# Performance work log

Hardware: AMD Instinct MI355X
Metric: run time of the kernel (lower is better)

## Reference

```python
import jax, jax.numpy as jnp
import numpy as np

DIM = 768
N_HEADS = 12
HEAD_DIM = DIM // N_HEADS
B, T = 2, 2048


def setup_inputs() -> dict:
    key = jax.random.key(0)
    ks = jax.random.split(key, 11)
    s = 0.02
    return {
        "q_in": jax.random.normal(ks[0], (B, T, DIM), jnp.float32),
        "k_in": jax.random.normal(ks[1], (B, T, DIM), jnp.float32),
        "v_in": jax.random.normal(ks[2], (B, T, DIM), jnp.float32),
        "Wq": jax.random.normal(ks[3], (DIM, DIM), jnp.float32) * s,
        "bq": jnp.zeros((DIM,), jnp.float32),
        "Wk": jax.random.normal(ks[4], (DIM, DIM), jnp.float32) * s,
        "bk": jnp.zeros((DIM,), jnp.float32),
        "Wv": jax.random.normal(ks[5], (DIM, DIM), jnp.float32) * s,
        "bv": jnp.zeros((DIM,), jnp.float32),
        "Wo": jax.random.normal(ks[6], (DIM, DIM), jnp.float32) * s,
        "bo": jnp.zeros((DIM,), jnp.float32),
    }


def reference(q_in, k_in, v_in, Wq, bq, Wk, bk, Wv, bv, Wo, bo):
    b, t, c = q_in.shape
    scale = HEAD_DIM ** -0.5
    # linear projections (torch Linear: x @ W.T + b)
    q = q_in @ Wq.T + bq
    k = k_in @ Wk.T + bk
    v = v_in @ Wv.T + bv
    # [b, t, h, d] -> [b, h, t, d]
    q = q.reshape(b, t, N_HEADS, HEAD_DIM).transpose(0, 2, 1, 3)
    k = k.reshape(b, t, N_HEADS, HEAD_DIM).transpose(0, 2, 1, 3)
    v = v.reshape(b, t, N_HEADS, HEAD_DIM).transpose(0, 2, 1, 3)
    scores = jnp.einsum("bhqd,bhkd->bhqk", q, k) * scale  # full TxT scores
    probs = jax.nn.softmax(scores, axis=-1)
    attn = jnp.einsum("bhqk,bhkd->bhqd", probs, v)
    attn = attn.transpose(0, 2, 1, 3).reshape(b, t, c)
    return attn @ Wo.T + bo
```

## Files before the change

### kernel.cpp

```cpp
#include <hip/hip_runtime.h>


typedef unsigned short u16;
typedef __attribute__((ext_vector_type(8))) short short8;
typedef __attribute__((ext_vector_type(4))) float float4v;

#define DIMC 768
#define NTOK 4096
#define NHD  12
#define HDD  64
#define SEQT 2048

__device__ __forceinline__ u16 f2bf(float f) {
  union { float f; unsigned u; } v; v.f = f;
  unsigned r = v.u + 0x7fffu + ((v.u >> 16) & 1u);
  return (u16)(r >> 16);
}
__device__ __forceinline__ float bf2f(u16 u) {
  union { unsigned u; float f; } v; v.u = ((unsigned)u) << 16;
  return v.f;
}

__global__ __launch_bounds__(256) void cvt3_kernel(
    const float* __restrict__ a, const float* __restrict__ b, const float* __restrict__ c,
    u16* __restrict__ oa, u16* __restrict__ ob, u16* __restrict__ oc) {
  int z = blockIdx.y;
  const float* s = (z == 0) ? a : (z == 1) ? b : c;
  u16* d = (z == 0) ? oa : (z == 1) ? ob : oc;
  size_t i = ((size_t)blockIdx.x * 256 + threadIdx.x) * 4;
  float4 v = *(const float4*)(s + i);
  *(ushort4*)(d + i) = make_ushort4(f2bf(v.x), f2bf(v.y), f2bf(v.z), f2bf(v.w));
}

__global__ __launch_bounds__(256) void cvt4_kernel(
    const float* __restrict__ a, const float* __restrict__ b,
    const float* __restrict__ c, const float* __restrict__ e,
    u16* __restrict__ oa, u16* __restrict__ ob, u16* __restrict__ oc, u16* __restrict__ oe) {
  int z = blockIdx.y;
  const float* s = (z == 0) ? a : (z == 1) ? b : (z == 2) ? c : e;
  u16* d = (z == 0) ? oa : (z == 1) ? ob : (z == 2) ? oc : oe;
  size_t i = ((size_t)blockIdx.x * 256 + threadIdx.x) * 4;
  float4 v = *(const float4*)(s + i);
  *(ushort4*)(d + i) = make_ushort4(f2bf(v.x), f2bf(v.y), f2bf(v.z), f2bf(v.w));
}

__device__ __forceinline__ void gemm_mainloop2(
    const u16* __restrict__ X, const u16* __restrict__ W,
    int m0, int n0, u16* Als, u16* Bls, float4v acc[4][2]) {
  int tid = threadIdx.x;
  int sr = tid >> 3, sc = (tid & 7) * 8;
  int w = tid >> 6, lane = tid & 63, quad = lane >> 4, r15 = lane & 15;
  int wm = (w >> 1) * 64, wn = (w & 1) * 32;
  const u16* xp0 = X + (size_t)(m0 + sr) * DIMC + sc;
  const u16* xp1 = xp0 + 32 * DIMC;
  const u16* xp2 = xp0 + 64 * DIMC;
  const u16* xp3 = xp0 + 96 * DIMC;
  const u16* wp0 = W + (size_t)(n0 + sr) * DIMC + sc;
  const u16* wp1 = wp0 + 32 * DIMC;
  uint4 pa0 = *(const uint4*)xp0, pa1 = *(const uint4*)xp1;
  uint4 pa2 = *(const uint4*)xp2, pa3 = *(const uint4*)xp3;
  uint4 pb0 = *(const uint4*)wp0, pb1 = *(const uint4*)wp1;
  for (int k0 = 0; k0 < DIMC; k0 += 64) {
    __syncthreads();
    *(uint4*)(Als + sr * 72 + sc) = pa0;
    *(uint4*)(Als + (sr + 32) * 72 + sc) = pa1;
    *(uint4*)(Als + (sr + 64) * 72 + sc) = pa2;
    *(uint4*)(Als + (sr + 96) * 72 + sc) = pa3;
    *(uint4*)(Bls + sr * 72 + sc) = pb0;
    *(uint4*)(Bls + (sr + 32) * 72 + sc) = pb1;
    __syncthreads();
    int kn = k0 + 64;
    if (kn < DIMC) {
      pa0 = *(const uint4*)(xp0 + kn); pa1 = *(const uint4*)(xp1 + kn);
      pa2 = *(const uint4*)(xp2 + kn); pa3 = *(const uint4*)(xp3 + kn);
      pb0 = *(const uint4*)(wp0 + kn); pb1 = *(const uint4*)(wp1 + kn);
    }
    #pragma unroll
    for (int sk = 0; sk < 2; sk++) {
      short8 af[4], bf[2];
      #pragma unroll
      for (int mf = 0; mf < 4; mf++)
        af[mf] = *(const short8*)(Als + (wm + mf * 16 + r15) * 72 + sk * 32 + quad * 8);
      #pragma unroll
      for (int nf = 0; nf < 2; nf++)
        bf[nf] = *(const short8*)(Bls + (wn + nf * 16 + r15) * 72 + sk * 32 + quad * 8);
      #pragma unroll
      for (int mf = 0; mf < 4; mf++)
        #pragma unroll
        for (int nf = 0; nf < 2; nf++)
          acc[mf][nf] = __builtin_amdgcn_mfma_f32_16x16x32_bf16(af[mf], bf[nf], acc[mf][nf], 0, 0, 0);
    }
  }
}

__global__ __launch_bounds__(256, 4) void gemm_qkv(
    const u16* __restrict__ xq, const u16* __restrict__ xk, const u16* __restrict__ xv,
    const u16* __restrict__ wq, const u16* __restrict__ wk, const u16* __restrict__ wv,
    const float* __restrict__ bq, const float* __restrict__ bk, const float* __restrict__ bv,
    u16* __restrict__ Qh, u16* __restrict__ Kh, u16* __restrict__ Vt) {
  __shared__ __align__(16) u16 Als[128 * 72];
  __shared__ __align__(16) u16 Bls[64 * 72];
  int z = blockIdx.z;
  const u16* X = (z == 0) ? xq : (z == 1) ? xk : xv;
  const u16* W = (z == 0) ? wq : (z == 1) ? wk : wv;
  const float* bias = (z == 0) ? bq : (z == 1) ? bk : bv;
  int m0 = blockIdx.x * 128, n0 = blockIdx.y * 64;
  float4v acc[4][2];
  #pragma unroll
  for (int i = 0; i < 4; i++)
    #pragma unroll
    for (int j = 0; j < 2; j++)
      #pragma unroll
      for (int r = 0; r < 4; r++) acc[i][j][r] = 0.f;
  gemm_mainloop2(X, W, m0, n0, Als, Bls, acc);
  int tid = threadIdx.x, w = tid >> 6, lane = tid & 63, quad = lane >> 4, r15 = lane & 15;
  int wm = (w >> 1) * 64, wn = (w & 1) * 32;
  #pragma unroll
  for (int mf = 0; mf < 4; mf++)
    #pragma unroll
    for (int nf = 0; nf < 2; nf++)
      #pragma unroll
      for (int rg = 0; rg < 4; rg++) {
        int m = m0 + wm + mf * 16 + quad * 4 + rg;
        int n = n0 + wn + nf * 16 + r15;
        float val = acc[mf][nf][rg] + bias[n];
        int b = m >> 11, t = m & 2047, h = n >> 6, d = n & 63;
        u16 o = f2bf(val);
        size_t bh = (size_t)(b * NHD + h);
        if (z == 2) Vt[(bh * HDD + d) * SEQT + t] = o;
        else if (z == 0) Qh[(bh * SEQT + t) * HDD + d] = o;
        else Kh[(bh * SEQT + t) * HDD + d] = o;
      }
}

__global__ __launch_bounds__(256, 3) void attn_kernel(
    const u16* __restrict__ Qh, const u16* __restrict__ Kh, const u16* __restrict__ Vt,
    u16* __restrict__ Opart, float* __restrict__ Lpart) {
  constexpr float CEXP = 0.125f * 1.44269504088896f;
  __shared__ __align__(16) u16 Kls[64 * 72];
  __shared__ __align__(16) u16 Vls[64 * 72];
  __shared__ __align__(16) u16 Pls[4 * 32 * 72];
  int bh = blockIdx.y, kv = blockIdx.z, qt0 = blockIdx.x * 128;
  int tid = threadIdx.x, w = tid >> 6, lane = tid & 63, quad = lane >> 4, r15 = lane & 15;
  int qw = qt0 + w * 32;

  short8 qa[2][2];
  #pragma unroll
  for (int qs = 0; qs < 2; qs++) {
    const u16* qp = Qh + ((size_t)bh * SEQT + qw + qs * 16 + r15) * HDD + quad * 8;
    qa[qs][0] = *(const short8*)qp;
    qa[qs][1] = *(const short8*)(qp + 32);
  }
  short8 ones;
  #pragma unroll
  for (int i = 0; i < 8; i++) ones[i] = (short)0x3F80;

  float4v oacc[2][4], lacc[2];
  #pragma unroll
  for (int qs = 0; qs < 2; qs++) {
    #pragma unroll
    for (int r = 0; r < 4; r++) lacc[qs][r] = 0.f;
    #pragma unroll
    for (int dt = 0; dt < 4; dt++)
      #pragma unroll
      for (int r = 0; r < 4; r++) oacc[qs][dt][r] = 0.f;
  }

  const u16* Kbase = Kh + (size_t)bh * SEQT * HDD;
  const u16* Vbase = Vt + (size_t)bh * HDD * SEQT;
  u16* Pw = Pls + w * (32 * 72);
  int sr = tid >> 3, sc = (tid & 7) * 8;
  int kt0 = kv * 1024;

  uint4 pk0 = *(const uint4*)(Kbase + (size_t)(kt0 + sr) * HDD + sc);
  uint4 pk1 = *(const uint4*)(Kbase + (size_t)(kt0 + sr + 32) * HDD + sc);
  uint4 pv0 = *(const uint4*)(Vbase + (size_t)sr * SEQT + kt0 + sc);
  uint4 pv1 = *(const uint4*)(Vbase + (size_t)(sr + 32) * SEQT + kt0 + sc);

  for (int it = 0; it < 16; it++) {
    __syncthreads();
    *(uint4*)(Kls + sr * 72 + sc) = pk0;
    *(uint4*)(Kls + (sr + 32) * 72 + sc) = pk1;
    *(uint4*)(Vls + sr * 72 + sc) = pv0;
    *(uint4*)(Vls + (sr + 32) * 72 + sc) = pv1;
    __syncthreads();
    int ktn = kt0 + ((it + 1) & 15) * 64;
    pk0 = *(const uint4*)(Kbase + (size_t)(ktn + sr) * HDD + sc);
    pk1 = *(const uint4*)(Kbase + (size_t)(ktn + sr + 32) * HDD + sc);
    pv0 = *(const uint4*)(Vbase + (size_t)sr * SEQT + ktn + sc);
    pv1 = *(const uint4*)(Vbase + (size_t)(sr + 32) * SEQT + ktn + sc);

    float4v st[4][2];
    #pragma unroll
    for (int nk = 0; nk < 4; nk++) {
      short8 k0 = *(const short8*)(Kls + (nk * 16 + r15) * 72 + quad * 8);
      short8 k1 = *(const short8*)(Kls + (nk * 16 + r15) * 72 + 32 + quad * 8);
      #pragma unroll
      for (int qs = 0; qs < 2; qs++) {
        float4v z;
        #pragma unroll
        for (int r = 0; r < 4; r++) z[r] = 0.f;
        z = __builtin_amdgcn_mfma_f32_16x16x32_bf16(k0, qa[qs][0], z, 0, 0, 0);
        z = __builtin_amdgcn_mfma_f32_16x16x32_bf16(k1, qa[qs][1], z, 0, 0, 0);
        st[nk][qs] = z;
      }
    }
    #pragma unroll
    for (int qs = 0; qs < 2; qs++)
      #pragma unroll
      for (int nk = 0; nk < 4; nk++) {
        float p0 = exp2f(st[nk][qs][0] * CEXP);
        float p1 = exp2f(st[nk][qs][1] * CEXP);
        float p2 = exp2f(st[nk][qs][2] * CEXP);
        float p3 = exp2f(st[nk][qs][3] * CEXP);
        unsigned lo = __builtin_amdgcn_perm(__float_as_uint(p1), __float_as_uint(p0), 0x07060302u);
        unsigned hi = __builtin_amdgcn_perm(__float_as_uint(p3), __float_as_uint(p2), 0x07060302u);
        *(uint2*)(Pw + (qs * 16 + r15) * 72 + nk * 16 + quad * 4) = make_uint2(lo, hi);
      }
    short8 pa[2][2];
    #pragma unroll
    for (int qs = 0; qs < 2; qs++) {
      pa[qs][0] = *(const short8*)(Pw + (qs * 16 + r15) * 72 + quad * 8);
      pa[qs][1] = *(const short8*)(Pw + (qs * 16 + r15) * 72 + 32 + quad * 8);
      lacc[qs] = __builtin_amdgcn_mfma_f32_16x16x32_bf16(pa[qs][0], ones, lacc[qs], 0, 0, 0);
      lacc[qs] = __builtin_amdgcn_mfma_f32_16x16x32_bf16(pa[qs][1], ones, lacc[qs], 0, 0, 0);
    }
    #pragma unroll
    for (int dt = 0; dt < 4; dt++) {
      short8 v0 = *(const short8*)(Vls + (dt * 16 + r15) * 72 + quad * 8);
      short8 v1 = *(const short8*)(Vls + (dt * 16 + r15) * 72 + 32 + quad * 8);
      #pragma unroll
      for (int qs = 0; qs < 2; qs++) {
        oacc[qs][dt] = __builtin_amdgcn_mfma_f32_16x16x32_bf16(pa[qs][0], v0, oacc[qs][dt], 0, 0, 0);
        oacc[qs][dt] = __builtin_amdgcn_mfma_f32_16x16x32_bf16(pa[qs][1], v1, oacc[qs][dt], 0, 0, 0);
      }
    }
  }
  size_t obase = ((size_t)kv * 2 * NHD + bh) * SEQT;
  #pragma unroll
  for (int qs = 0; qs < 2; qs++)
    #pragma unroll
    for (int rg = 0; rg < 4; rg++) {
      int q = qw + qs * 16 + quad * 4 + rg;
      u16* orow = Opart + (obase + q) * HDD;
      #pragma unroll
      for (int dt = 0; dt < 4; dt++) orow[dt * 16 + r15] = f2bf(oacc[qs][dt][rg]);
      if (r15 == 0) Lpart[obase + q] = lacc[qs][rg];
    }
}

__global__ __launch_bounds__(256) void merge_kernel(
    const u16* __restrict__ Opart, const float* __restrict__ Lpart, u16* __restrict__ X2) {
  int tid = threadIdx.x;
  int row = blockIdx.x * 32 + (tid >> 3);
  int dcol = (tid & 7) * 8;
  int bh = row >> 11, t = row & 2047;
  size_t off1 = (size_t)row * HDD + dcol;
  size_t off2 = off1 + (size_t)2 * NHD * SEQT * HDD;
  ushort4 a0 = *(const ushort4*)(Opart + off1);
  ushort4 a1 = *(const ushort4*)(Opart + off1 + 4);
  ushort4 b0 = *(const ushort4*)(Opart + off2);
  ushort4 b1 = *(const ushort4*)(Opart + off2 + 4);
  float inv = 1.0f / (Lpart[row] + Lpart[row + 2 * NHD * SEQT]);
  int b = bh / NHD, h = bh % NHD;
  u16 o[8];
  o[0] = f2bf((bf2f(a0.x) + bf2f(b0.x)) * inv);
  o[1] = f2bf((bf2f(a0.y) + bf2f(b0.y)) * inv);
  o[2] = f2bf((bf2f(a0.z) + bf2f(b0.z)) * inv);
  o[3] = f2bf((bf2f(a0.w) + bf2f(b0.w)) * inv);
  o[4] = f2bf((bf2f(a1.x) + bf2f(b1.x)) * inv);
  o[5] = f2bf((bf2f(a1.y) + bf2f(b1.y)) * inv);
  o[6] = f2bf((bf2f(a1.z) + bf2f(b1.z)) * inv);
  o[7] = f2bf((bf2f(a1.w) + bf2f(b1.w)) * inv);
  *(uint4*)(X2 + ((size_t)b * SEQT + t) * DIMC + h * HDD + dcol) = *(uint4*)o;
}

__global__ __launch_bounds__(256, 4) void gemm_out(
    const u16* __restrict__ X2, const u16* __restrict__ wo,
    const float* __restrict__ bo, float* __restrict__ out) {
  __shared__ __align__(16) u16 Als[128 * 72];
  __shared__ __align__(16) u16 Bls[64 * 72];
  int m0 = blockIdx.x * 128, n0 = blockIdx.y * 64;
  float4v acc[4][2];
  #pragma unroll
  for (int i = 0; i < 4; i++)
    #pragma unroll
    for (int j = 0; j < 2; j++)
      #pragma unroll
      for (int r = 0; r < 4; r++) acc[i][j][r] = 0.f;
  gemm_mainloop2(X2, wo, m0, n0, Als, Bls, acc);
  int tid = threadIdx.x, w = tid >> 6, lane = tid & 63, quad = lane >> 4, r15 = lane & 15;
  int wm = (w >> 1) * 64, wn = (w & 1) * 32;
  #pragma unroll
  for (int mf = 0; mf < 4; mf++)
    #pragma unroll
    for (int nf = 0; nf < 2; nf++)
      #pragma unroll
      for (int rg = 0; rg < 4; rg++) {
        int m = m0 + wm + mf * 16 + quad * 4 + rg;
        int n = n0 + wn + nf * 16 + r15;
        out[(size_t)m * DIMC + n] = acc[mf][nf][rg] + bo[n];
      }
}

extern "C" void kernel_launch(void* const* d_in, const int* in_sizes, int n_in,
                              void* d_out, int out_size, void* d_ws, size_t ws_size,
                              hipStream_t stream) {
  const float* q_in = (const float*)d_in[0];
  const float* k_in = (const float*)d_in[1];
  const float* v_in = (const float*)d_in[2];
  const float* Wq = (const float*)d_in[3];
  const float* bq = (const float*)d_in[4];
  const float* Wk = (const float*)d_in[5];
  const float* bk = (const float*)d_in[6];
  const float* Wv = (const float*)d_in[7];
  const float* bv = (const float*)d_in[8];
  const float* Wo = (const float*)d_in[9];
  const float* bo = (const float*)d_in[10];

  const size_t NX = (size_t)NTOK * DIMC;
  const size_t NW = (size_t)DIMC * DIMC;
  u16* ws = (u16*)d_ws;
  u16* qb = ws;
  u16* kb = qb + NX;
  u16* vb = kb + NX;
  u16* wqb = vb + NX;
  u16* wkb = wqb + NW;
  u16* wvb = wkb + NW;
  u16* wob = wvb + NW;
  u16* Qh = wob + NW;
  u16* Kh = Qh + NX;
  u16* Vt = Kh + NX;
  u16* X2 = Vt + NX;
  u16* Opart = qb;
  float* Lpart = (float*)(ws + 2 * NX);

  cvt3_kernel<<<dim3(NX / 1024, 3), 256, 0, stream>>>(q_in, k_in, v_in, qb, kb, vb);
  cvt4_kernel<<<dim3(NW / 1024, 4), 256, 0, stream>>>(Wq, Wk, Wv, Wo, wqb, wkb, wvb, wob);
  gemm_qkv<<<dim3(NTOK / 128, DIMC / 64, 3), 256, 0, stream>>>(
      qb, kb, vb, wqb, wkb, wvb, bq, bk, bv, Qh, Kh, Vt);
  attn_kernel<<<dim3(SEQT / 128, 2 * NHD, 2), 256, 0, stream>>>(Qh, Kh, Vt, Opart, Lpart);
  merge_kernel<<<dim3(2 * NHD * SEQT / 32), 256, 0, stream>>>(Opart, Lpart, X2);
  gemm_out<<<dim3(NTOK / 128, DIMC / 64), 256, 0, stream>>>(X2, wob, bo, (float*)d_out);
}
```

Measured before the change: 200.3 us.

## Fold softmax scale into Q projection and double attention KV tile to 128

The Q projection epilogue now multiplies by scale*log2(e), so the attention kernel can call the raw hardware exp2 with no per-element multiply. The attention loop stages 128 keys per iteration instead of 64, halving the number of barriers and loop trips, and processes the tile in two 64-key halves. The P buffer is unchanged, and a shared zero accumulator replaces the per-iteration zeroing. This raises LDS use (bigger K and V tiles) and register pressure from more prefetch registers, which could reduce occupancy below the 3 blocks per CU requested in the launch bounds.

```diff
diff --git a/kernel.cpp b/kernel.cpp
--- a/kernel.cpp
+++ b/kernel.cpp
@@ -124,6 +124,7 @@
         int m = m0 + wm + mf * 16 + quad * 4 + rg;
         int n = n0 + wn + nf * 16 + r15;
         float val = acc[mf][nf][rg] + bias[n];
+        if (z == 0) val *= 0.180336880f;
         int b = m >> 11, t = m & 2047, h = n >> 6, d = n & 63;
         u16 o = f2bf(val);
         size_t bh = (size_t)(b * NHD + h);
@@ -136,9 +137,8 @@
 __global__ __launch_bounds__(256, 3) void attn_kernel(
     const u16* __restrict__ Qh, const u16* __restrict__ Kh, const u16* __restrict__ Vt,
     u16* __restrict__ Opart, float* __restrict__ Lpart) {
-  constexpr float CEXP = 0.125f * 1.44269504088896f;
-  __shared__ __align__(16) u16 Kls[64 * 72];
-  __shared__ __align__(16) u16 Vls[64 * 72];
+  __shared__ __align__(16) u16 Kls[128 * 72];
+  __shared__ __align__(16) u16 Vls[64 * 136];
   __shared__ __align__(16) u16 Pls[4 * 32 * 72];
   int bh = blockIdx.y, kv = blockIdx.z, qt0 = blockIdx.x * 128;
   int tid = threadIdx.x, w = tid >> 6, lane = tid & 63, quad = lane >> 4, r15 = lane & 15;
@@ -154,6 +154,9 @@
   short8 ones;
   #pragma unroll
   for (int i = 0; i < 8; i++) ones[i] = (short)0x3F80;
+  float4v fzero;
+  #pragma unroll
+  for (int r = 0; r < 4; r++) fzero[r] = 0.f;
 
   float4v oacc[2][4], lacc[2];
   #pragma unroll
@@ -169,70 +172,77 @@
   const u16* Kbase = Kh + (size_t)bh * SEQT * HDD;
   const u16* Vbase = Vt + (size_t)bh * HDD * SEQT;
   u16* Pw = Pls + w * (32 * 72);
-  int sr = tid >> 3, sc = (tid & 7) * 8;
+  int krow = tid >> 3, kcol = (tid & 7) * 8;
+  int vrow = tid >> 4, vcol = (tid & 15) * 8;
   int kt0 = kv * 1024;
 
-  uint4 pk0 = *(const uint4*)(Kbase + (size_t)(kt0 + sr) * HDD + sc);
-  uint4 pk1 = *(const uint4*)(Kbase + (size_t)(kt0 + sr + 32) * HDD + sc);
-  uint4 pv0 = *(const uint4*)(Vbase + (size_t)sr * SEQT + kt0 + sc);
-  uint4 pv1 = *(const uint4*)(Vbase + (size_t)(sr + 32) * SEQT + kt0 + sc);
-
-  for (int it = 0; it < 16; it++) {
+  uint4 pk[4], pv[4];
+  #pragma unroll
+  for (int p = 0; p < 4; p++) {
+    pk[p] = *(const uint4*)(Kbase + (size_t)(kt0 + krow + p * 32) * HDD + kcol);
+    pv[p] = *(const uint4*)(Vbase + (size_t)(vrow + p * 16) * SEQT + kt0 + vcol);
+  }
+
+  for (int it = 0; it < 8; it++) {
     __syncthreads();
-    *(uint4*)(Kls + sr * 72 + sc) = pk0;
-    *(uint4*)(Kls + (sr + 32) * 72 + sc) = pk1;
-    *(uint4*)(Vls + sr * 72 + sc) = pv0;
-    *(uint4*)(Vls + (sr + 32) * 72 + sc) = pv1;
+    #pragma unroll
+    for (int p = 0; p < 4; p++) {
+      *(uint4*)(Kls + (krow + p * 32) * 72 + kcol) = pk[p];
+      *(uint4*)(Vls + (vrow + p * 16) * 136 + vcol) = pv[p];
+    }
     __syncthreads();
-    int ktn = kt0 + ((it + 1) & 15) * 64;
-    pk0 = *(const uint4*)(Kbase + (size_t)(ktn + sr) * HDD + sc);
-    pk1 = *(const uint4*)(Kbase + (size_t)(ktn + sr + 32) * HDD + sc);
-    pv0 = *(const uint4*)(Vbase + (size_t)sr * SEQT + ktn + sc);
-    pv1 = *(const uint4*)(Vbase + (size_t)(sr + 32) * SEQT + ktn + sc);
-
-    float4v st[4][2];
-    #pragma unroll
-    for (int nk = 0; nk < 4; nk++) {
-      short8 k0 = *(const short8*)(Kls + (nk * 16 + r15) * 72 + quad * 8);
-      short8 k1 = *(const short8*)(Kls + (nk * 16 + r15) * 72 + 32 + quad * 8);
+    int ktn = kt0 + ((it + 1) & 7) * 128;
+    #pragma unroll
+    for (int p = 0; p < 4; p++) {
+      pk[p] = *(const uint4*)(Kbase + (size_t)(ktn + krow + p * 32) * HDD + kcol);
+      pv[p] = *(const uint4*)(Vbase + (size_t)(vrow + p * 16) * SEQT + ktn + vcol);
+    }
+
+    #pragma unroll
+    for (int h = 0; h < 2; h++) {
+      float4v st[4][2];
+      #pragma unroll
+      for (int nk = 0; nk < 4; nk++) {
+        const u16* kp = Kls + (h * 64 + nk * 16 + r15) * 72 + quad * 8;
+        short8 k0 = *(const short8*)kp;
+        short8 k1 = *(const short8*)(kp + 32);
+        #pragma unroll
+        for (int qs = 0; qs < 2; qs++) {
+          float4v z = __builtin_amdgcn_mfma_f32_16x16x32_bf16(k0, qa[qs][0], fzero, 0, 0, 0);
+          z = __builtin_amdgcn_mfma_f32_16x16x32_bf16(k1, qa[qs][1], z, 0, 0, 0);
+          st[nk][qs] = z;
+        }
+      }
+      #pragma unroll
+      for (int qs = 0; qs < 2; qs++)
+        #pragma unroll
+        for (int nk = 0; nk < 4; nk++) {
+          float p0 = __builtin_amdgcn_exp2f(st[nk][qs][0]);
+          float p1 = __builtin_amdgcn_exp2f(st[nk][qs][1]);
+          float p2 = __builtin_amdgcn_exp2f(st[nk][qs][2]);
+          float p3 = __builtin_amdgcn_exp2f(st[nk][qs][3]);
+          unsigned lo = __builtin_amdgcn_perm(__float_as_uint(p1), __float_as_uint(p0), 0x07060302u);
+          unsigned hi = __builtin_amdgcn_perm(__float_as_uint(p3), __float_as_uint(p2), 0x07060302u);
+          *(uint2*)(Pw + (qs * 16 + r15) * 72 + nk * 16 + quad * 4) = make_uint2(lo, hi);
+        }
+      short8 pa[2][2];
       #pragma unroll
       for (int qs = 0; qs < 2; qs++) {
-        float4v z;
+        pa[qs][0] = *(const short8*)(Pw + (qs * 16 + r15) * 72 + quad * 8);
+        pa[qs][1] = *(const short8*)(Pw + (qs * 16 + r15) * 72 + 32 + quad * 8);
+        lacc[qs] = __builtin_amdgcn_mfma_f32_16x16x32_bf16(pa[qs][0], ones, lacc[qs], 0, 0, 0);
+        lacc[qs] = __builtin_amdgcn_mfma_f32_16x16x32_bf16(pa[qs][1], ones, lacc[qs], 0, 0, 0);
+      }
+      #pragma unroll
+      for (int dt = 0; dt < 4; dt++) {
+        const u16* vp = Vls + (dt * 16 + r15) * 136 + h * 64 + quad * 8;
+        short8 v0 = *(const short8*)vp;
+        short8 v1 = *(const short8*)(vp + 32);
         #pragma unroll
-        for (int r = 0; r < 4; r++) z[r] = 0.f;
-        z = __builtin_amdgcn_mfma_f32_16x16x32_bf16(k0, qa[qs][0], z, 0, 0, 0);
-        z = __builtin_amdgcn_mfma_f32_16x16x32_bf16(k1, qa[qs][1], z, 0, 0, 0);
-        st[nk][qs] = z;
-      }
-    }
-    #pragma unroll
-    for (int qs = 0; qs < 2; qs++)
-      #pragma unroll
-      for (int nk = 0; nk < 4; nk++) {
-        float p0 = exp2f(st[nk][qs][0] * CEXP);
-        float p1 = exp2f(st[nk][qs][1] * CEXP);
-        float p2 = exp2f(st[nk][qs][2] * CEXP);
-        float p3 = exp2f(st[nk][qs][3] * CEXP);
-        unsigned lo = __builtin_amdgcn_perm(__float_as_uint(p1), __float_as_uint(p0), 0x07060302u);
-        unsigned hi = __builtin_amdgcn_perm(__float_as_uint(p3), __float_as_uint(p2), 0x07060302u);
-        *(uint2*)(Pw + (qs * 16 + r15) * 72 + nk * 16 + quad * 4) = make_uint2(lo, hi);
-      }
-    short8 pa[2][2];
-    #pragma unroll
-    for (int qs = 0; qs < 2; qs++) {
-      pa[qs][0] = *(const short8*)(Pw + (qs * 16 + r15) * 72 + quad * 8);
-      pa[qs][1] = *(const short8*)(Pw + (qs * 16 + r15) * 72 + 32 + quad * 8);
-      lacc[qs] = __builtin_amdgcn_mfma_f32_16x16x32_bf16(pa[qs][0], ones, lacc[qs], 0, 0, 0);
-      lacc[qs] = __builtin_amdgcn_mfma_f32_16x16x32_bf16(pa[qs][1], ones, lacc[qs], 0, 0, 0);
-    }
-    #pragma unroll
-    for (int dt = 0; dt < 4; dt++) {
-      short8 v0 = *(const short8*)(Vls + (dt * 16 + r15) * 72 + quad * 8);
-      short8 v1 = *(const short8*)(Vls + (dt * 16 + r15) * 72 + 32 + quad * 8);
-      #pragma unroll
-      for (int qs = 0; qs < 2; qs++) {
-        oacc[qs][dt] = __builtin_amdgcn_mfma_f32_16x16x32_bf16(pa[qs][0], v0, oacc[qs][dt], 0, 0, 0);
-        oacc[qs][dt] = __builtin_amdgcn_mfma_f32_16x16x32_bf16(pa[qs][1], v1, oacc[qs][dt], 0, 0, 0);
+        for (int qs = 0; qs < 2; qs++) {
+          oacc[qs][dt] = __builtin_amdgcn_mfma_f32_16x16x32_bf16(pa[qs][0], v0, oacc[qs][dt], 0, 0, 0);
+          oacc[qs][dt] = __builtin_amdgcn_mfma_f32_16x16x32_bf16(pa[qs][1], v1, oacc[qs][dt], 0, 0, 0);
+        }
       }
     }
   }
```

New measurement: 268.5 us. 34.1% more time.

## Split attention KV into three chunks, coalesce V transpose, fold softmax scale into Q

Applied to the files above, without the earlier changes.

The attention grid now splits the 32 key tiles into three uneven chunks (11/11/10) instead of two, with occupancy hint raised to 4, and the merge kernel sums three partials. The QKV GEMM stages the V tile through shared memory so the transposed Vt writes become 16-byte coalesced stores instead of scattered 2-byte ones. The softmax scale times log2(e) is folded into Q at projection time, so the attention kernel can call the raw exp2 builtin with no per-element multiply. The trade-offs are a wave-quantization change from the new grid size, extra partial traffic in merge, and Lpart relocated into the dead Wq buffer.

```diff
diff --git a/kernel.cpp b/kernel.cpp
--- a/kernel.cpp
+++ b/kernel.cpp
@@ -115,34 +115,59 @@
   gemm_mainloop2(X, W, m0, n0, Als, Bls, acc);
   int tid = threadIdx.x, w = tid >> 6, lane = tid & 63, quad = lane >> 4, r15 = lane & 15;
   int wm = (w >> 1) * 64, wn = (w & 1) * 32;
-  #pragma unroll
-  for (int mf = 0; mf < 4; mf++)
-    #pragma unroll
-    for (int nf = 0; nf < 2; nf++)
-      #pragma unroll
-      for (int rg = 0; rg < 4; rg++) {
-        int m = m0 + wm + mf * 16 + quad * 4 + rg;
-        int n = n0 + wn + nf * 16 + r15;
-        float val = acc[mf][nf][rg] + bias[n];
-        int b = m >> 11, t = m & 2047, h = n >> 6, d = n & 63;
-        u16 o = f2bf(val);
-        size_t bh = (size_t)(b * NHD + h);
-        if (z == 2) Vt[(bh * HDD + d) * SEQT + t] = o;
-        else if (z == 0) Qh[(bh * SEQT + t) * HDD + d] = o;
-        else Kh[(bh * SEQT + t) * HDD + d] = o;
-      }
-}
-
-__global__ __launch_bounds__(256, 3) void attn_kernel(
+  if (z == 2) {
+    __syncthreads();
+    u16* T = Als;
+    #pragma unroll
+    for (int mf = 0; mf < 4; mf++)
+      #pragma unroll
+      for (int nf = 0; nf < 2; nf++)
+        #pragma unroll
+        for (int rg = 0; rg < 4; rg++) {
+          int mloc = wm + mf * 16 + quad * 4 + rg;
+          int nloc = wn + nf * 16 + r15;
+          T[nloc * 136 + mloc] = f2bf(acc[mf][nf][rg] + bias[n0 + nloc]);
+        }
+    __syncthreads();
+    int d = tid >> 2, seg = tid & 3;
+    int b = m0 >> 11, t0 = m0 & 2047, h = n0 >> 6;
+    size_t base = (((size_t)(b * NHD + h)) * HDD + d) * SEQT + t0 + seg * 32;
+    const u16* src = T + d * 136 + seg * 32;
+    #pragma unroll
+    for (int j = 0; j < 4; j++)
+      *(uint4*)(Vt + base + j * 8) = *(const uint4*)(src + j * 8);
+  } else {
+    #pragma unroll
+    for (int mf = 0; mf < 4; mf++)
+      #pragma unroll
+      for (int nf = 0; nf < 2; nf++)
+        #pragma unroll
+        for (int rg = 0; rg < 4; rg++) {
+          int m = m0 + wm + mf * 16 + quad * 4 + rg;
+          int n = n0 + wn + nf * 16 + r15;
+          float val = acc[mf][nf][rg] + bias[n];
+          if (z == 0) val *= 0.180336880f;
+          int b = m >> 11, t = m & 2047, h = n >> 6, d = n & 63;
+          u16 o = f2bf(val);
+          size_t bh = (size_t)(b * NHD + h);
+          if (z == 0) Qh[(bh * SEQT + t) * HDD + d] = o;
+          else Kh[(bh * SEQT + t) * HDD + d] = o;
+        }
+  }
+}
+
+__global__ __launch_bounds__(256, 4) void attn_kernel(
     const u16* __restrict__ Qh, const u16* __restrict__ Kh, const u16* __restrict__ Vt,
     u16* __restrict__ Opart, float* __restrict__ Lpart) {
-  constexpr float CEXP = 0.125f * 1.44269504088896f;
   __shared__ __align__(16) u16 Kls[64 * 72];
   __shared__ __align__(16) u16 Vls[64 * 72];
   __shared__ __align__(16) u16 Pls[4 * 32 * 72];
-  int bh = blockIdx.y, kv = blockIdx.z, qt0 = blockIdx.x * 128;
+  int bh = blockIdx.y, sp = blockIdx.z, qt0 = blockIdx.x * 128;
   int tid = threadIdx.x, w = tid >> 6, lane = tid & 63, quad = lane >> 4, r15 = lane & 15;
   int qw = qt0 + w * 32;
+  int tile0 = (sp < 2) ? sp * 11 : 22;
+  int nt = (sp < 2) ? 11 : 10;
+  int kt0 = tile0 * 64;
 
   short8 qa[2][2];
   #pragma unroll
@@ -154,6 +179,9 @@
   short8 ones;
   #pragma unroll
   for (int i = 0; i < 8; i++) ones[i] = (short)0x3F80;
+  float4v fzero;
+  #pragma unroll
+  for (int r = 0; r < 4; r++) fzero[r] = 0.f;
 
   float4v oacc[2][4], lacc[2];
   #pragma unroll
@@ -170,21 +198,21 @@
   const u16* Vbase = Vt + (size_t)bh * HDD * SEQT;
   u16* Pw = Pls + w * (32 * 72);
   int sr = tid >> 3, sc = (tid & 7) * 8;
-  int kt0 = kv * 1024;
 
   uint4 pk0 = *(const uint4*)(Kbase + (size_t)(kt0 + sr) * HDD + sc);
   uint4 pk1 = *(const uint4*)(Kbase + (size_t)(kt0 + sr + 32) * HDD + sc);
   uint4 pv0 = *(const uint4*)(Vbase + (size_t)sr * SEQT + kt0 + sc);
   uint4 pv1 = *(const uint4*)(Vbase + (size_t)(sr + 32) * SEQT + kt0 + sc);
 
-  for (int it = 0; it < 16; it++) {
+  for (int it = 0; it < nt; it++) {
     __syncthreads();
     *(uint4*)(Kls + sr * 72 + sc) = pk0;
     *(uint4*)(Kls + (sr + 32) * 72 + sc) = pk1;
     *(uint4*)(Vls + sr * 72 + sc) = pv0;
     *(uint4*)(Vls + (sr + 32) * 72 + sc) = pv1;
     __syncthreads();
-    int ktn = kt0 + ((it + 1) & 15) * 64;
+    int nit = it + 1; if (nit == nt) nit = 0;
+    int ktn = kt0 + nit * 64;
     pk0 = *(const uint4*)(Kbase + (size_t)(ktn + sr) * HDD + sc);
     pk1 = *(const uint4*)(Kbase + (size_t)(ktn + sr + 32) * HDD + sc);
     pv0 = *(const uint4*)(Vbase + (size_t)sr * SEQT + ktn + sc);
@@ -197,10 +225,7 @@
       short8 k1 = *(const short8*)(Kls + (nk * 16 + r15) * 72 + 32 + quad * 8);
       #pragma unroll
       for (int qs = 0; qs < 2; qs++) {
-        float4v z;
-        #pragma unroll
-        for (int r = 0; r < 4; r++) z[r] = 0.f;
-        z = __builtin_amdgcn_mfma_f32_16x16x32_bf16(k0, qa[qs][0], z, 0, 0, 0);
+        float4v z = __builtin_amdgcn_mfma_f32_16x16x32_bf16(k0, qa[qs][0], fzero, 0, 0, 0);
         z = __builtin_amdgcn_mfma_f32_16x16x32_bf16(k1, qa[qs][1], z, 0, 0, 0);
         st[nk][qs] = z;
       }
@@ -209,10 +234,10 @@
     for (int qs = 0; qs < 2; qs++)
       #pragma unroll
       for (int nk = 0; nk < 4; nk++) {
-        float p0 = exp2f(st[nk][qs][0] * CEXP);
-        float p1 = exp2f(st[nk][qs][1] * CEXP);
-        float p2 = exp2f(st[nk][qs][2] * CEXP);
-        float p3 = exp2f(st[nk][qs][3] * CEXP);
+        float p0 = __builtin_amdgcn_exp2f(st[nk][qs][0]);
+        float p1 = __builtin_amdgcn_exp2f(st[nk][qs][1]);
+        float p2 = __builtin_amdgcn_exp2f(st[nk][qs][2]);
+        float p3 = __builtin_amdgcn_exp2f(st[nk][qs][3]);
         unsigned lo = __builtin_amdgcn_perm(__float_as_uint(p1), __float_as_uint(p0), 0x07060302u);
         unsigned hi = __builtin_amdgcn_perm(__float_as_uint(p3), __float_as_uint(p2), 0x07060302u);
         *(uint2*)(Pw + (qs * 16 + r15) * 72 + nk * 16 + quad * 4) = make_uint2(lo, hi);
@@ -236,7 +261,7 @@
       }
     }
   }
-  size_t obase = ((size_t)kv * 2 * NHD + bh) * SEQT;
+  size_t obase = ((size_t)sp * 2 * NHD + bh) * SEQT;
   #pragma unroll
   for (int qs = 0; qs < 2; qs++)
     #pragma unroll
@@ -251,27 +276,26 @@
 
 __global__ __launch_bounds__(256) void merge_kernel(
     const u16* __restrict__ Opart, const float* __restrict__ Lpart, u16* __restrict__ X2) {
+  const size_t NXe = (size_t)2 * NHD * SEQT * HDD;
+  const size_t LS = (size_t)2 * NHD * SEQT;
   int tid = threadIdx.x;
   int row = blockIdx.x * 32 + (tid >> 3);
   int dcol = (tid & 7) * 8;
   int bh = row >> 11, t = row & 2047;
-  size_t off1 = (size_t)row * HDD + dcol;
-  size_t off2 = off1 + (size_t)2 * NHD * SEQT * HDD;
-  ushort4 a0 = *(const ushort4*)(Opart + off1);
-  ushort4 a1 = *(const ushort4*)(Opart + off1 + 4);
-  ushort4 b0 = *(const ushort4*)(Opart + off2);
-  ushort4 b1 = *(const ushort4*)(Opart + off2 + 4);
-  float inv = 1.0f / (Lpart[row] + Lpart[row + 2 * NHD * SEQT]);
+  size_t off = (size_t)row * HDD + dcol;
+  float inv = 1.0f / (Lpart[row] + Lpart[row + LS] + Lpart[row + 2 * LS]);
   int b = bh / NHD, h = bh % NHD;
   u16 o[8];
-  o[0] = f2bf((bf2f(a0.x) + bf2f(b0.x)) * inv);
-  o[1] = f2bf((bf2f(a0.y) + bf2f(b0.y)) * inv);
-  o[2] = f2bf((bf2f(a0.z) + bf2f(b0.z)) * inv);
-  o[3] = f2bf((bf2f(a0.w) + bf2f(b0.w)) * inv);
-  o[4] = f2bf((bf2f(a1.x) + bf2f(b1.x)) * inv);
-  o[5] = f2bf((bf2f(a1.y) + bf2f(b1.y)) * inv);
-  o[6] = f2bf((bf2f(a1.z) + bf2f(b1.z)) * inv);
-  o[7] = f2bf((bf2f(a1.w) + bf2f(b1.w)) * inv);
+  #pragma unroll
+  for (int half = 0; half < 2; half++) {
+    ushort4 a = *(const ushort4*)(Opart + off + half * 4);
+    ushort4 c = *(const ushort4*)(Opart + off + NXe + half * 4);
+    ushort4 e = *(const ushort4*)(Opart + off + 2 * NXe + half * 4);
+    o[half * 4 + 0] = f2bf((bf2f(a.x) + bf2f(c.x) + bf2f(e.x)) * inv);
+    o[half * 4 + 1] = f2bf((bf2f(a.y) + bf2f(c.y) + bf2f(e.y)) * inv);
+    o[half * 4 + 2] = f2bf((bf2f(a.z) + bf2f(c.z) + bf2f(e.z)) * inv);
+    o[half * 4 + 3] = f2bf((bf2f(a.w) + bf2f(c.w) + bf2f(e.w)) * inv);
+  }
   *(uint4*)(X2 + ((size_t)b * SEQT + t) * DIMC + h * HDD + dcol) = *(uint4*)o;
 }
 
@@ -333,13 +357,13 @@
   u16* Vt = Kh + NX;
   u16* X2 = Vt + NX;
   u16* Opart = qb;
-  float* Lpart = (float*)(ws + 2 * NX);
+  float* Lpart = (float*)wqb;
 
   cvt3_kernel<<<dim3(NX / 1024, 3), 256, 0, stream>>>(q_in, k_in, v_in, qb, kb, vb);
   cvt4_kernel<<<dim3(NW / 1024, 4), 256, 0, stream>>>(Wq, Wk, Wv, Wo, wqb, wkb, wvb, wob);
   gemm_qkv<<<dim3(NTOK / 128, DIMC / 64, 3), 256, 0, stream>>>(
       qb, kb, vb, wqb, wkb, wvb, bq, bk, bv, Qh, Kh, Vt);
-  attn_kernel<<<dim3(SEQT / 128, 2 * NHD, 2), 256, 0, stream>>>(Qh, Kh, Vt, Opart, Lpart);
+  attn_kernel<<<dim3(SEQT / 128, 2 * NHD, 3), 256, 0, stream>>>(Qh, Kh, Vt, Opart, Lpart);
   merge_kernel<<<dim3(2 * NHD * SEQT / 32), 256, 0, stream>>>(Opart, Lpart, X2);
   gemm_out<<<dim3(NTOK / 128, DIMC / 64), 256, 0, stream>>>(X2, wob, bo, (float*)d_out);
 }
```

Result: faster. 190.9 us (-4.7%).
